# Optimization experiments

Measured on AMD Instinct MI355X. Metric: run time of the kernel, lower is better.

The kernel has to match this reference:

```python
import jax, jax.numpy as jnp
import numpy as np

N, E = 3200, 50000
RBF, HID = 16, 128
CUT = 5.0
NS, NV = 32, 16            # multiplicities of 0e and 1o blocks
D = NS + 3 * NV            # 80 = node/message irrep dim
WNUM = NS*NS + NV*NS + NS*NV + NV*NV  # 2304 tensor-product weights per edge
EPS = 1e-8
# path normalization (fully-connected TP, 2 paths per output irrep)
A1 = 1.0 / np.sqrt(2.0 * NS)
A2 = 1.0 / np.sqrt(2.0 * NV)
A3 = 1.0 / np.sqrt(2.0 * NS)
A4 = 1.0 / np.sqrt(2.0 * NV)
ISQ3 = 1.0 / np.sqrt(3.0)


def setup_inputs() -> dict:
    key = jax.random.key(0)
    ks = jax.random.split(key, 24)
    nrm = lambda k, s, sc=1.0: jax.random.normal(k, s, jnp.float32) * sc
    x = nrm(ks[0], (N, D))
    edge_src = jax.random.randint(ks[1], (E,), 0, N)
    edge_dst = jax.random.randint(ks[2], (E,), 0, N)
    dirs = nrm(ks[3], (E, 3))
    unit = dirs / jnp.linalg.norm(dirs, axis=1, keepdims=True)
    # component-normalized SH for l=0,1: [1, sqrt(3)*r_hat]
    edge_sh = jnp.concatenate([jnp.ones((E, 1), jnp.float32), np.sqrt(3.0) * unit], axis=1)
    edge_rbf = nrm(ks[4], (E, RBF))
    edge_len = jax.random.uniform(ks[5], (E,), jnp.float32, 0.1, 6.0)  # some beyond cutoff
    inp = dict(x=x, edge_src=edge_src, edge_dst=edge_dst, edge_sh=edge_sh,
               edge_rbf=edge_rbf, edge_len=edge_len)
    # IrrepNorm affine params
    inp['norm_w'] = jnp.ones((D,), jnp.float32)
    inp['norm_b'] = jnp.zeros((D,), jnp.float32)
    # radial weight MLP (RBF -> HID -> HID -> WNUM)
    inp['mw1'] = nrm(ks[6], (RBF, HID), 1.0/np.sqrt(RBF)); inp['mb1'] = jnp.zeros((HID,), jnp.float32)
    inp['mw2'] = nrm(ks[7], (HID, HID), 1.0/np.sqrt(HID)); inp['mb2'] = jnp.zeros((HID,), jnp.float32)
    inp['mw3'] = nrm(ks[8], (HID, WNUM), 1.0/np.sqrt(HID)); inp['mb3'] = jnp.zeros((WNUM,), jnp.float32)
    # edge gate MLP (RBF -> HID -> 1)
    inp['gw1'] = nrm(ks[9], (RBF, HID), 1.0/np.sqrt(RBF)); inp['gb1'] = jnp.zeros((HID,), jnp.float32)
    inp['gw2'] = nrm(ks[10], (HID, 1), 1.0/np.sqrt(HID)); inp['gb2'] = jnp.zeros((1,), jnp.float32)
    # equivariant linears (e3nn stores N(0,1) weights, normalizes by 1/sqrt(fan_in))
    inp['Ws'] = nrm(ks[11], (NS, NS + NV))   # msg_linear scalar part: 32 -> 32 scalars + 16 gates
    inp['Wv'] = nrm(ks[12], (NV, NV))        # msg_linear vector part
    inp['Us'] = nrm(ks[13], (NS, NS))        # update_linear
    inp['Uv'] = nrm(ks[14], (NV, NV))
    inp['Ss'] = nrm(ks[15], (NS, NS))        # self_linear
    inp['Sv'] = nrm(ks[16], (NV, NV))
    inp['res_scale'] = jnp.float32(0.1)
    return inp


def _irrep_norm(x, w, b):
    s = x[:, :NS]
    v = x[:, NS:].reshape(-1, NV, 3)
    mean = s.mean(axis=1, keepdims=True)
    var = ((s - mean) ** 2).mean(axis=1, keepdims=True)
    s = (s - mean) / jnp.sqrt(var + EPS)
    rms = jnp.sqrt((v ** 2).mean(axis=2, keepdims=True) + EPS)
    v = v / rms
    out = jnp.concatenate([s, v.reshape(-1, 3 * NV)], axis=-1)
    return out * w + b


def reference(x, edge_src, edge_dst, edge_sh, edge_rbf, edge_len,
              norm_w, norm_b, mw1, mb1, mw2, mb2, mw3, mb3,
              gw1, gb1, gw2, gb2, Ws, Wv, Us, Uv, Ss, Sv, res_scale):
    silu = jax.nn.silu
    x_norm = _irrep_norm(x, norm_w, norm_b)                  # [N, 80]
    # radial tensor-product weights per edge
    h = silu(edge_rbf @ mw1 + mb1)
    h = silu(h @ mw2 + mb2)
    tpw = h @ mw3 + mb3                                      # [E, 2304]
    o1 = NS*NS; o2 = o1 + NV*NS; o3 = o2 + NS*NV
    w1 = tpw[:, :o1].reshape(-1, NS, NS)
    w2 = tpw[:, o1:o2].reshape(-1, NV, NS)
    w3 = tpw[:, o2:o3].reshape(-1, NS, NV)
    w4 = tpw[:, o3:].reshape(-1, NV, NV)
    # gather source node features
    xs = x_norm[edge_src, :NS]                               # [E, 32]
    xv = x_norm[edge_src, NS:].reshape(-1, NV, 3)            # [E, 16, 3]
    sh0 = edge_sh[:, 0]                                      # [E]
    sh1 = edge_sh[:, 1:4]                                    # [E, 3]
    # fully-connected TP paths
    msg_s = A1 * jnp.einsum('ei,eio->eo', xs * sh0[:, None], w1)
    inner = jnp.einsum('eim,em->ei', xv, sh1) * ISQ3         # 1o x 1o -> 0e
    msg_s = msg_s + A2 * jnp.einsum('ei,eio->eo', inner, w2)
    msg_v = A3 * jnp.einsum('ei,eio->eo', xs, w3)[:, :, None] * sh1[:, None, :]
    msg_v = msg_v + A4 * jnp.einsum('eim,eio->eom', xv, w4) * sh0[:, None, None]
    m = jnp.concatenate([msg_s, msg_v.reshape(-1, 3 * NV)], axis=-1)  # [E, 80]
    # cutoff envelope and learned edge gate
    cutoff_w = 0.5 * (jnp.cos(jnp.pi * edge_len / CUT) + 1.0) * (edge_len <= CUT).astype(x.dtype)
    gate_w = jax.nn.sigmoid(silu(edge_rbf @ gw1 + gb1) @ gw2 + gb2)   # [E, 1]
    edge_w = cutoff_w[:, None] * gate_w                               # [E, 1]
    m = m * edge_w
    # scatter-add aggregate + normalization
    agg = jax.ops.segment_sum(m, edge_dst, num_segments=N)            # [N, 80]
    den = jax.ops.segment_sum(edge_w, edge_dst, num_segments=N)       # [N, 1]
    agg = agg / jnp.maximum(den, 1e-8)
    # msg_linear -> scalars + gates + gated vectors
    ag_s = agg[:, :NS]
    ag_v = agg[:, NS:].reshape(-1, NV, 3)
    sc = (ag_s @ Ws) / np.sqrt(NS)                                    # [N, 48]
    vc = jnp.einsum('nim,io->nom', ag_v, Wv) / np.sqrt(NV)            # [N, 16, 3]
    s_g = silu(sc[:, :NS])
    gates = jax.nn.sigmoid(sc[:, NS:])
    v_g = vc * gates[:, :, None]
    # update + self interaction
    upd_s = (s_g @ Us) / np.sqrt(NS)
    upd_v = jnp.einsum('nim,io->nom', v_g, Uv) / np.sqrt(NV)
    self_s = (x_norm[:, :NS] @ Ss) / np.sqrt(NS)
    self_v = jnp.einsum('nim,io->nom', x_norm[:, NS:].reshape(-1, NV, 3), Sv) / np.sqrt(NV)
    out = jnp.concatenate([self_s + upd_s, (self_v + upd_v).reshape(-1, 3 * NV)], axis=-1)
    return x + res_scale * out
```

## Files before the change

### kernel.cpp

```cpp
#include <hip/hip_runtime.h>
#include <hip/hip_bf16.h>
#include <math.h>

#define N_NODES 3200
#define E_EDGES 50000
#define RBFN 16
#define HID 128
#define NS 32
#define NV 16
#define DD 80
#define WNUM 2304
#define CUTF 5.0f
#define EPSF 1e-8f

#define A1C 0.125f
#define A2C 0.17677669529663687f
#define A3C 0.125f
#define A4C 0.17677669529663687f
#define A2ISQ 0.10206207261596575f

typedef __attribute__((ext_vector_type(4))) float f32x4;
typedef __attribute__((ext_vector_type(8))) short bf16x8;

__device__ __forceinline__ float sigm(float x) { return 1.0f / (1.0f + __expf(-x)); }
__device__ __forceinline__ float silu_f(float x) { return x * sigm(x); }

__device__ __forceinline__ short bf16r(float x) {
    union { float f; unsigned u; } v; v.f = x;
    unsigned r = (v.u + 0x7fffu + ((v.u >> 16) & 1u)) >> 16;
    return (short)r;
}
__device__ __forceinline__ float b2f(unsigned short s) {
    union { float f; unsigned u; } v; v.u = ((unsigned)s) << 16; return v.f;
}

__global__ void k_scan(const int* __restrict__ hist, int* __restrict__ start) {
    __shared__ int part[256];
    int t = threadIdx.x;
    int loc[13];
    int s = 0;
#pragma unroll
    for (int j = 0; j < 13; j++) {
        int idx = t * 13 + j;
        int v = (idx < N_NODES) ? hist[idx] : 0;
        loc[j] = s; s += v;
    }
    part[t] = s;
    __syncthreads();
    for (int off = 1; off < 256; off <<= 1) {
        int v = part[t];
        int add = (t >= off) ? part[t - off] : 0;
        __syncthreads();
        part[t] = v + add;
        __syncthreads();
    }
    int pre = (t == 0) ? 0 : part[t - 1];
#pragma unroll
    for (int j = 0; j < 13; j++) {
        int idx = t * 13 + j;
        if (idx < N_NODES) start[idx] = pre + loc[j];
    }
    if (t == 255) start[N_NODES] = part[255];
}

__global__ void k_scatter(const int* __restrict__ edst, const int* __restrict__ start,
                          int* __restrict__ cur, int* __restrict__ perm) {
    int e = blockIdx.x * 256 + threadIdx.x;
    if (e < E_EDGES) {
        int d = edst[e];
        int pos = start[d] + atomicAdd(&cur[d], 1);
        perm[pos] = e;
    }
}

__global__ void k_prep0(const float* __restrict__ mw2, __hip_bfloat16* __restrict__ mw2f) {
    __shared__ __hip_bfloat16 st[2048];
    int t = blockIdx.x, tid = threadIdx.x;
    for (int idx = tid; idx < 2048; idx += 256) {
        int k = idx >> 4, c = idx & 15;
        float v = mw2[k * HID + t * 16 + c];
        int kk = k >> 5, q4 = (k >> 3) & 3, j = k & 7;
        st[kk * 512 + (q4 * 16 + c) * 8 + j] = __float2bfloat16(v);
    }
    __syncthreads();
    ((bf16x8*)(mw2f + t * 2048))[tid] = ((const bf16x8*)st)[tid];
}

__global__ __launch_bounds__(256) void k_front(
    const float* __restrict__ rbf, const float* __restrict__ elen,
    const int* __restrict__ edst,
    const float* __restrict__ mw1, const float* __restrict__ mb1,
    const float* __restrict__ gw1, const float* __restrict__ gb1,
    const float* __restrict__ gw2, const float* __restrict__ gb2,
    const float* __restrict__ mb2, const __hip_bfloat16* __restrict__ mw2f,
    const float* __restrict__ mw3, const float* __restrict__ mb3,
    const float* __restrict__ x, const float* __restrict__ nw, const float* __restrict__ nb,
    float* __restrict__ ewg, __hip_bfloat16* __restrict__ h2b,
    __hip_bfloat16* __restrict__ mw3f, __hip_bfloat16* __restrict__ biasf,
    float* __restrict__ xn, int* __restrict__ hist) {
    __shared__ __align__(16) char smem[16640];
    int b = blockIdx.x, tid = threadIdx.x;
    if (b < 782) {
        __hip_bfloat16* h1l = (__hip_bfloat16*)smem;
        int wid = __builtin_amdgcn_readfirstlane(tid >> 6);
        int lane = tid & 63;
        int base = b * 64;
        int eb = base + wid * 16;
        {
            int c0 = lane, c1 = 64 + lane;
            float t0[16], t1[16], g0[16], g1[16];
            float b0 = mb1[c0], b1 = mb1[c1], gb0v = gb1[c0], gb1v = gb1[c1];
#pragma unroll
            for (int e = 0; e < 16; e++) { t0[e] = b0; t1[e] = b1; g0[e] = gb0v; g1[e] = gb1v; }
#pragma unroll
            for (int r = 0; r < RBFN; r++) {
                float w0 = mw1[r * HID + c0], w1 = mw1[r * HID + c1];
                float v0 = gw1[r * HID + c0], v1 = gw1[r * HID + c1];
#pragma unroll
                for (int e = 0; e < 16; e++) {
                    int ee = eb + e; if (ee >= E_EDGES) ee = E_EDGES - 1;
                    float rv = rbf[ee * RBFN + r];
                    t0[e] += rv * w0; t1[e] += rv * w1;
                    g0[e] += rv * v0; g1[e] += rv * v1;
                }
            }
            float q0 = gw2[c0], q1 = gw2[c1];
            float gb2v = gb2[0];
#pragma unroll
            for (int e = 0; e < 16; e++) {
                int le = wid * 16 + e;
                h1l[le * 128 + c0] = __float2bfloat16(silu_f(t0[e]));
                h1l[le * 128 + c1] = __float2bfloat16(silu_f(t1[e]));
                float p = silu_f(g0[e]) * q0 + silu_f(g1[e]) * q1;
                p += __shfl_xor(p, 1);  p += __shfl_xor(p, 2);  p += __shfl_xor(p, 4);
                p += __shfl_xor(p, 8);  p += __shfl_xor(p, 16); p += __shfl_xor(p, 32);
                if (lane == 0 && eb + e < E_EDGES) {
                    float len = elen[eb + e];
                    float cut = (len <= CUTF) ? 0.5f * (cosf(3.14159265358979f * len / CUTF) + 1.0f) : 0.f;
                    ewg[eb + e] = cut * sigm(p + gb2v);
                }
            }
        }
        __syncthreads();
        {
            int q4 = lane >> 4, l15 = lane & 15;
            int le = wid * 16 + l15;
            bf16x8 af[4];
#pragma unroll
            for (int kk = 0; kk < 4; kk++)
                af[kk] = *(const bf16x8*)(h1l + le * 128 + kk * 32 + q4 * 8);
            const f32x4 zf = {0.f, 0.f, 0.f, 0.f};
#pragma unroll
            for (int ct = 0; ct < 8; ct++) {
                f32x4 acc = zf;
#pragma unroll
                for (int kk = 0; kk < 4; kk++) {
                    bf16x8 bw = *(const bf16x8*)(mw2f + (ct * 4 + kk) * 512 + lane * 8);
                    acc = __builtin_amdgcn_mfma_f32_16x16x32_bf16(af[kk], bw, acc, 0, 0, 0);
                }
                float bias = mb2[ct * 16 + l15];
#pragma unroll
                for (int r = 0; r < 4; r++) {
                    int ge = base + wid * 16 + q4 * 4 + r;
                    if (ge < E_EDGES)
                        h2b[ge * HID + ct * 16 + l15] = __float2bfloat16(silu_f(acc[r] + bias));
                }
            }
        }
    } else if (b < 927) {
        int b2 = b - 782;
        __hip_bfloat16* st = (__hip_bfloat16*)smem;
        if (b2 < 144) {
            for (int idx = tid; idx < 2048; idx += 256) {
                int k = idx >> 4, c = idx & 15;
                float v = mw3[k * WNUM + b2 * 16 + c];
                int kk = k >> 5, q4 = (k >> 3) & 3, j = k & 7;
                st[kk * 512 + (q4 * 16 + c) * 8 + j] = __float2bfloat16(v);
            }
            __syncthreads();
            ((bf16x8*)(mw3f + b2 * 2048))[tid] = ((const bf16x8*)st)[tid];
        } else {
            for (int idx = tid; idx < 3072; idx += 256) {
                float val;
                if (idx < 1024) {
                    int oh = idx >> 9, l = (idx >> 3) & 63, j = idx & 7;
                    int o = oh * 16 + (l & 15), i = (l >> 4) * 8 + j;
                    val = mb3[i * 32 + o];
                } else if (idx < 2048) {
                    int t = idx - 1024;
                    int oh = t >> 9, l = (t >> 3) & 63, j = t & 7;
                    int o = oh * 16 + (l & 15), i = (l >> 4) * 8 + j;
                    val = (i < 16) ? mb3[1024 + i * 32 + o] : 0.f;
                } else if (idx < 2560) {
                    int t = idx - 2048;
                    int l = t >> 3, j = t & 7;
                    int o = l & 15, i = (l >> 4) * 8 + j;
                    val = mb3[1536 + i * 16 + o];
                } else {
                    int t = idx - 2560;
                    int l = t >> 3, j = t & 7;
                    int o = l & 15, i = (l >> 4) * 8 + j;
                    val = (i < 16) ? mb3[2048 + i * 16 + o] : 0.f;
                }
                biasf[idx] = __float2bfloat16(val);
            }
        }
    } else if (b < 1727) {
        float* row = (float*)smem;
        int sub = tid >> 6, t = tid & 63;
        int n = (b - 927) * 4 + sub;
        float* rw = row + sub * 80;
        const float* xr = x + n * DD;
        rw[t] = xr[t];
        if (t < 16) rw[64 + t] = xr[64 + t];
        __syncthreads();
        float mean = 0.f;
#pragma unroll
        for (int i = 0; i < NS; i++) mean += rw[i];
        mean *= (1.0f / NS);
        float var = 0.f;
#pragma unroll
        for (int i = 0; i < NS; i++) { float d = rw[i] - mean; var += d * d; }
        var *= (1.0f / NS);
        float inv = rsqrtf(var + EPSF);
        if (t < NS) xn[n * DD + t] = (rw[t] - mean) * inv * nw[t] + nb[t];
        if (t < 48) {
            int j = t / 3;
            float v0 = rw[NS + 3 * j], v1 = rw[NS + 3 * j + 1], v2 = rw[NS + 3 * j + 2];
            float rms = sqrtf((v0 * v0 + v1 * v1 + v2 * v2) * (1.0f / 3.0f) + EPSF);
            xn[n * DD + NS + t] = rw[NS + t] / rms * nw[NS + t] + nb[NS + t];
        }
    } else {
        int e = (b - 1727) * 256 + tid;
        if (e < E_EDGES) atomicAdd(&hist[edst[e]], 1);
    }
}

__global__ __launch_bounds__(128) void k_msg(
    const float* __restrict__ xn, const __hip_bfloat16* __restrict__ h2b,
    const float* __restrict__ ewg, const int* __restrict__ esrc,
    const int* __restrict__ edst, const int* __restrict__ perm,
    const float* __restrict__ esh,
    const __hip_bfloat16* __restrict__ mw3f, const __hip_bfloat16* __restrict__ biasf,
    const int* __restrict__ startp, float* __restrict__ agg, float* __restrict__ den) {
    __shared__ __align__(16) char pool[29696];
    unsigned short (*xng)[82]  = (unsigned short(*)[82])(pool);
    unsigned short (*innr)[16] = (unsigned short(*)[16])(pool + 20992);
    float (*sh1l)[4] = (float(*)[4])(pool + 25088);
    float* sh0l = (float*)(pool + 27136);
    float* ewl  = (float*)(pool + 27648);
    int* dstl   = (int*)(pool + 28160);
    int* srcl   = (int*)(pool + 28672);
    int* gel    = (int*)(pool + 29184);
    float* msgl = (float*)pool;

    const int tid = threadIdx.x;
    const int wid = __builtin_amdgcn_readfirstlane(tid >> 6);
    const int lane = tid & 63;
    const int q4 = lane >> 4;
    const int l15 = lane & 15;
    const int ib = q4 * 8;
    const int role = blockIdx.x & 1;
    const int e0 = (blockIdx.x >> 1) * 128;

    if (tid < 128) {
        int slot = e0 + tid;
        bool v = slot < E_EDGES;
        int ge = v ? perm[slot] : 0;
        gel[tid] = ge;
        srcl[tid] = esrc[ge];
        dstl[tid] = v ? edst[ge] : -1;
        ewl[tid] = v ? ewg[ge] : 0.f;
        sh0l[tid] = esh[ge * 4];
        sh1l[tid][0] = esh[ge * 4 + 1];
        sh1l[tid][1] = esh[ge * 4 + 2];
        sh1l[tid][2] = esh[ge * 4 + 3];
    }
    __syncthreads();
    for (int idx = tid; idx < 128 * 80; idx += 128) {
        int e = idx / 80, q = idx - e * 80;
        xng[e][q] = (unsigned short)bf16r(xn[srcl[e] * 80 + q]);
    }
    __syncthreads();
    for (int idx = tid; idx < 128 * 16; idx += 128) {
        int e = idx >> 4, i = idx & 15;
        float d = b2f(xng[e][32 + 3 * i]) * sh1l[e][0]
                + b2f(xng[e][32 + 3 * i + 1]) * sh1l[e][1]
                + b2f(xng[e][32 + 3 * i + 2]) * sh1l[e][2];
        innr[e][i] = (unsigned short)bf16r(A2ISQ * d);
    }
    __syncthreads();

    int el[4];
#pragma unroll
    for (int et = 0; et < 4; et++) el[et] = wid * 64 + et * 16 + l15;
    bf16x8 hfr[4][4];
#pragma unroll
    for (int et = 0; et < 4; et++) {
        int ge = gel[el[et]];
        const __hip_bfloat16* hr = h2b + ge * HID;
#pragma unroll
        for (int kk = 0; kk < 4; kk++)
            hfr[et][kk] = *(const bf16x8*)(hr + kk * 32 + ib);
    }
    const f32x4 zf = {0.f, 0.f, 0.f, 0.f};
    const bf16x8* gp = (const bf16x8*)mw3f;
    int cnt = E_EDGES - e0; if (cnt > 128) cnt = 128;

    if (role == 0) {
        float f1[4];
        f32x4 msgS[2][4];
#pragma unroll
        for (int et = 0; et < 4; et++) {
            f1[et] = A1C * sh0l[el[et]];
            bf16x8 p18, p28;
#pragma unroll
            for (int j = 0; j < 8; j++) {
                p18[j] = bf16r(b2f(xng[el[et]][ib + j]) * f1[et]);
                p28[j] = (ib + j < 16) ? (short)innr[el[et]][ib + j] : (short)0;
            }
            bf16x8 ba1a = *(const bf16x8*)(biasf + lane * 8);
            bf16x8 ba1b = *(const bf16x8*)(biasf + 512 + lane * 8);
            bf16x8 ba2a = *(const bf16x8*)(biasf + 1024 + lane * 8);
            bf16x8 ba2b = *(const bf16x8*)(biasf + 1536 + lane * 8);
            f32x4 a0 = __builtin_amdgcn_mfma_f32_16x16x32_bf16(ba1a, p18, zf, 0, 0, 0);
            msgS[0][et] = __builtin_amdgcn_mfma_f32_16x16x32_bf16(ba2a, p28, a0, 0, 0, 0);
            f32x4 a1 = __builtin_amdgcn_mfma_f32_16x16x32_bf16(ba1b, p18, zf, 0, 0, 0);
            msgS[1][et] = __builtin_amdgcn_mfma_f32_16x16x32_bf16(ba2b, p28, a1, 0, 0, 0);
        }
        auto computeA = [&](int n, bf16x8 (&A)[8]) {
            f32x4 acc[2][4];
#pragma unroll
            for (int half = 0; half < 2; half++)
#pragma unroll
                for (int et = 0; et < 4; et++) acc[half][et] = zf;
#pragma unroll
            for (int half = 0; half < 2; half++)
#pragma unroll
                for (int kk = 0; kk < 4; kk++)
#pragma unroll
                    for (int et = 0; et < 4; et++)
                        acc[half][et] = __builtin_amdgcn_mfma_f32_16x16x32_bf16(
                            A[half * 4 + kk], hfr[et][kk], acc[half][et], 0, 0, 0);
            float p[4];
            if (n < 32) {
#pragma unroll
                for (int et = 0; et < 4; et++) p[et] = f1[et] * b2f(xng[el[et]][n]);
            } else {
#pragma unroll
                for (int et = 0; et < 4; et++) p[et] = b2f(innr[el[et]][n - 32]);
            }
#pragma unroll
            for (int half = 0; half < 2; half++)
#pragma unroll
                for (int et = 0; et < 4; et++)
#pragma unroll
                    for (int r = 0; r < 4; r++)
                        msgS[half][et][r] += p[et] * acc[half][et][r];
        };
        bf16x8 A0[8], A1[8];
#pragma unroll
        for (int f = 0; f < 8; f++) A0[f] = gp[f * 64 + lane];
        for (int n = 0; n < 48; n += 2) {
            const bf16x8* g1 = gp + (n + 1) * 512;
#pragma unroll
            for (int f = 0; f < 8; f++) A1[f] = g1[f * 64 + lane];
            computeA(n, A0);
            if (n + 2 < 48) {
                const bf16x8* g2 = gp + (n + 2) * 512;
#pragma unroll
                for (int f = 0; f < 8; f++) A0[f] = g2[f * 64 + lane];
            }
            computeA(n + 1, A1);
        }
        __syncthreads();
#pragma unroll
        for (int et = 0; et < 4; et++) {
            int le = el[et];
            float ew = ewl[le];
#pragma unroll
            for (int oh = 0; oh < 2; oh++)
#pragma unroll
                for (int r = 0; r < 4; r++)
                    msgl[le * 48 + oh * 16 + q4 * 4 + r] = msgS[oh][et][r] * ew;
        }
        __syncthreads();
        if (tid < 33) {
            int c = tid;
            int cur = dstl[0];
            float acc = 0.f;
            for (int r = 0; r < cnt; r++) {
                int nd = dstl[r];
                if (nd != cur) {
                    if (cur >= 0) {
                        bool interior = (startp[cur] >= e0) && (startp[cur + 1] <= e0 + 128);
                        float* p = (c == 32) ? (den + cur) : (agg + cur * 80 + c);
                        if (interior) *p = acc; else atomicAdd(p, acc);
                    }
                    acc = 0.f; cur = nd;
                }
                acc += (c == 32) ? ewl[r] : msgl[r * 48 + c];
            }
            if (cur >= 0) {
                bool interior = (startp[cur] >= e0) && (startp[cur + 1] <= e0 + 128);
                float* p = (c == 32) ? (den + cur) : (agg + cur * 80 + c);
                if (interior) *p = acc; else atomicAdd(p, acc);
            }
        }
    } else {
        float f4e[4];
        f32x4 q3[4], qv[3][4];
#pragma unroll
        for (int et = 0; et < 4; et++) {
            f4e[et] = A4C * sh0l[el[et]];
            bf16x8 xs8;
#pragma unroll
            for (int j = 0; j < 8; j++) xs8[j] = (short)xng[el[et]][ib + j];
            bf16x8 ba3 = *(const bf16x8*)(biasf + 2048 + lane * 8);
            bf16x8 ba4 = *(const bf16x8*)(biasf + 2560 + lane * 8);
            q3[et] = __builtin_amdgcn_mfma_f32_16x16x32_bf16(ba3, xs8, zf, 0, 0, 0);
#pragma unroll
            for (int m = 0; m < 3; m++) {
                bf16x8 t8;
#pragma unroll
                for (int j = 0; j < 8; j++) {
                    int i = ib + j;
                    t8[j] = (i < 16) ? (short)xng[el[et]][32 + 3 * i + m] : (short)0;
                }
                qv[m][et] = __builtin_amdgcn_mfma_f32_16x16x32_bf16(ba4, t8, zf, 0, 0, 0);
            }
        }
        auto computeB = [&](int n, bf16x8 (&A)[8]) {
            f32x4 acc[2][4];
#pragma unroll
            for (int half = 0; half < 2; half++)
#pragma unroll
                for (int et = 0; et < 4; et++) acc[half][et] = zf;
#pragma unroll
            for (int half = 0; half < 2; half++)
#pragma unroll
                for (int kk = 0; kk < 4; kk++)
#pragma unroll
                    for (int et = 0; et < 4; et++)
                        acc[half][et] = __builtin_amdgcn_mfma_f32_16x16x32_bf16(
                            A[half * 4 + kk], hfr[et][kk], acc[half][et], 0, 0, 0);
            if (n < 64) {
#pragma unroll
                for (int half = 0; half < 2; half++) {
                    int i = 2 * (n - 48) + half;
                    float p[4];
#pragma unroll
                    for (int et = 0; et < 4; et++) p[et] = b2f(xng[el[et]][i]);
#pragma unroll
                    for (int et = 0; et < 4; et++)
#pragma unroll
                        for (int r = 0; r < 4; r++)
                            q3[et][r] += p[et] * acc[half][et][r];
                }
            } else {
#pragma unroll
                for (int half = 0; half < 2; half++) {
                    int i = 2 * (n - 64) + half;
#pragma unroll
                    for (int m = 0; m < 3; m++) {
                        float p[4];
#pragma unroll
                        for (int et = 0; et < 4; et++) p[et] = b2f(xng[el[et]][32 + 3 * i + m]);
#pragma unroll
                        for (int et = 0; et < 4; et++)
#pragma unroll
                            for (int r = 0; r < 4; r++)
                                qv[m][et][r] += p[et] * acc[half][et][r];
                    }
                }
            }
        };
        bf16x8 A0[8], A1[8];
#pragma unroll
        for (int f = 0; f < 8; f++) A0[f] = gp[48 * 512 + f * 64 + lane];
        for (int n = 48; n < 72; n += 2) {
            const bf16x8* g1 = gp + (n + 1) * 512;
#pragma unroll
            for (int f = 0; f < 8; f++) A1[f] = g1[f * 64 + lane];
            computeB(n, A0);
            if (n + 2 < 72) {
                const bf16x8* g2 = gp + (n + 2) * 512;
#pragma unroll
                for (int f = 0; f < 8; f++) A0[f] = g2[f * 64 + lane];
            }
            computeB(n + 1, A1);
        }
        __syncthreads();
#pragma unroll
        for (int et = 0; et < 4; et++) {
            int le = el[et];
            float ew = ewl[le];
            float s0 = sh1l[le][0], s1 = sh1l[le][1], s2 = sh1l[le][2];
            float b4 = f4e[et];
#pragma unroll
            for (int r = 0; r < 4; r++) {
                int o = q4 * 4 + r;
                float qq = A3C * q3[et][r];
                msgl[le * 48 + o * 3 + 0] = (qq * s0 + b4 * qv[0][et][r]) * ew;
                msgl[le * 48 + o * 3 + 1] = (qq * s1 + b4 * qv[1][et][r]) * ew;
                msgl[le * 48 + o * 3 + 2] = (qq * s2 + b4 * qv[2][et][r]) * ew;
            }
        }
        __syncthreads();
        if (tid < 48) {
            int c = tid;
            int cur = dstl[0];
            float acc = 0.f;
            for (int r = 0; r < cnt; r++) {
                int nd = dstl[r];
                if (nd != cur) {
                    if (cur >= 0) {
                        bool interior = (startp[cur] >= e0) && (startp[cur + 1] <= e0 + 128);
                        float* p = agg + cur * 80 + 32 + c;
                        if (interior) *p = acc; else atomicAdd(p, acc);
                    }
                    acc = 0.f; cur = nd;
                }
                acc += msgl[r * 48 + c];
            }
            if (cur >= 0) {
                bool interior = (startp[cur] >= e0) && (startp[cur + 1] <= e0 + 128);
                float* p = agg + cur * 80 + 32 + c;
                if (interior) *p = acc; else atomicAdd(p, acc);
            }
        }
    }
}

__global__ void k_update(
    const float* __restrict__ x, const float* __restrict__ xn,
    const float* __restrict__ agg, const float* __restrict__ den,
    const float* __restrict__ Ws, const float* __restrict__ Wv,
    const float* __restrict__ Us, const float* __restrict__ Uv,
    const float* __restrict__ Ss, const float* __restrict__ Sv,
    const float* __restrict__ rsp, float* __restrict__ out) {
    int n = blockIdx.x, t = threadIdx.x;
    __shared__ float ag[DD];
    __shared__ float xnl[DD];
    __shared__ float sg[NS];
    __shared__ float gt[NV];
    __shared__ float vg[48];
    float idv = 1.0f / fmaxf(den[n], 1e-8f);
    ag[t] = agg[n * DD + t] * idv;
    if (t < 16) ag[64 + t] = agg[n * DD + 64 + t] * idv;
    xnl[t] = xn[n * DD + t];
    if (t < 16) xnl[64 + t] = xn[n * DD + 64 + t];
    __syncthreads();
    const float iqs = 0.17677669529663687f;
    const float iqv = 0.25f;
    if (t < 48) {
        float acc = 0.f;
#pragma unroll
        for (int i = 0; i < NS; i++) acc += ag[i] * Ws[i * 48 + t];
        acc *= iqs;
        if (t < NS) sg[t] = silu_f(acc);
        else gt[t - NS] = sigm(acc);
    }
    __syncthreads();
    if (t < 48) {
        int o = t / 3, m = t - 3 * o;
        float acc = 0.f;
#pragma unroll
        for (int i = 0; i < NV; i++) acc += ag[NS + 3 * i + m] * Wv[i * NV + o];
        vg[t] = acc * iqv * gt[o];
    }
    __syncthreads();
    float rs = rsp[0];
    if (t < NS) {
        float us = 0.f, ss = 0.f;
#pragma unroll
        for (int i = 0; i < NS; i++) { us += sg[i] * Us[i * NS + t]; ss += xnl[i] * Ss[i * NS + t]; }
        out[n * DD + t] = x[n * DD + t] + rs * ((ss + us) * iqs);
    }
    if (t < 48) {
        int o = t / 3, m = t - 3 * o;
        float uv = 0.f, sv = 0.f;
#pragma unroll
        for (int i = 0; i < NV; i++) { uv += vg[3 * i + m] * Uv[i * NV + o]; sv += xnl[NS + 3 * i + m] * Sv[i * NV + o]; }
        out[n * DD + NS + t] = x[n * DD + NS + t] + rs * ((sv + uv) * iqv);
    }
}

extern "C" void kernel_launch(void* const* d_in, const int* in_sizes, int n_in,
                              void* d_out, int out_size, void* d_ws, size_t ws_size,
                              hipStream_t stream) {
    (void)in_sizes; (void)n_in; (void)out_size; (void)ws_size;
    const float* x    = (const float*)d_in[0];
    const int*   esrc = (const int*)d_in[1];
    const int*   edst = (const int*)d_in[2];
    const float* esh  = (const float*)d_in[3];
    const float* erbf = (const float*)d_in[4];
    const float* elen = (const float*)d_in[5];
    const float* nw   = (const float*)d_in[6];
    const float* nb   = (const float*)d_in[7];
    const float* mw1  = (const float*)d_in[8];
    const float* mb1  = (const float*)d_in[9];
    const float* mw2  = (const float*)d_in[10];
    const float* mb2  = (const float*)d_in[11];
    const float* mw3  = (const float*)d_in[12];
    const float* mb3  = (const float*)d_in[13];
    const float* gw1  = (const float*)d_in[14];
    const float* gb1  = (const float*)d_in[15];
    const float* gw2  = (const float*)d_in[16];
    const float* gb2  = (const float*)d_in[17];
    const float* Ws   = (const float*)d_in[18];
    const float* Wv   = (const float*)d_in[19];
    const float* Us   = (const float*)d_in[20];
    const float* Uv   = (const float*)d_in[21];
    const float* Ss   = (const float*)d_in[22];
    const float* Sv   = (const float*)d_in[23];
    const float* rsp  = (const float*)d_in[24];
    float* out = (float*)d_out;
    float* ws  = (float*)d_ws;

    float* agg    = ws;
    float* den    = ws + 256000;
    int*   hist   = (int*)(ws + 259200);
    int*   cur    = (int*)(ws + 262400);
    int*   startp = (int*)(ws + 265600);
    int*   perm   = (int*)(ws + 268801);
    float* xn     = ws + 318804;
    float* ewg    = ws + 574804;
    __hip_bfloat16* h2b   = (__hip_bfloat16*)(ws + 624804);
    __hip_bfloat16* mw3f  = (__hip_bfloat16*)(ws + 3824804);
    __hip_bfloat16* biasf = (__hip_bfloat16*)(ws + 3972260);
    __hip_bfloat16* mw2f  = (__hip_bfloat16*)(ws + 3973796);

    hipMemsetAsync(ws, 0, 265600 * sizeof(float), stream);
    k_prep0<<<8, 256, 0, stream>>>(mw2, mw2f);
    k_front<<<1923, 256, 0, stream>>>(erbf, elen, edst, mw1, mb1, gw1, gb1, gw2, gb2,
                                      mb2, mw2f, mw3, mb3, x, nw, nb,
                                      ewg, h2b, mw3f, biasf, xn, hist);
    k_scan<<<1, 256, 0, stream>>>(hist, startp);
    k_scatter<<<196, 256, 0, stream>>>(edst, startp, cur, perm);
    k_msg<<<782, 128, 0, stream>>>(xn, h2b, ewg, esrc, edst, perm, esh,
                                   mw3f, biasf, startp, agg, den);
    k_update<<<N_NODES, 64, 0, stream>>>(x, xn, agg, den, Ws, Wv, Us, Uv, Ss, Sv, rsp, out);
}
```

Baseline: 269.4 us.

## Split message kernel weight-row loop across six blocks per edge tile

The message kernel previously used two blocks per 128-edge tile (scalar and vector outputs), each looping over 48 or 24 weight rows. It now launches six blocks per tile, each handling 12 weight rows, and gathers only the node-feature columns its slice needs. The segmented reduction is spread over both waves and always uses atomics because partial sums now come from several blocks. This gives more parallelism on a grid that had only 782 blocks. In exchange, the h2b fragment loads and source gathers are repeated per slice, and atomic traffic on agg rises.

```diff
diff --git a/kernel.cpp b/kernel.cpp
--- a/kernel.cpp
+++ b/kernel.cpp
@@ -260,8 +260,9 @@
     const int q4 = lane >> 4;
     const int l15 = lane & 15;
     const int ib = q4 * 8;
-    const int role = blockIdx.x & 1;
-    const int e0 = (blockIdx.x >> 1) * 128;
+    const int grp = blockIdx.x / 6;
+    const int slice = blockIdx.x - 6 * grp;
+    const int e0 = grp * 128;
 
     if (tid < 128) {
         int slot = e0 + tid;
@@ -277,17 +278,49 @@
         sh1l[tid][2] = esh[ge * 4 + 3];
     }
     __syncthreads();
-    for (int idx = tid; idx < 128 * 80; idx += 128) {
-        int e = idx / 80, q = idx - e * 80;
-        xng[e][q] = (unsigned short)bf16r(xn[srcl[e] * 80 + q]);
-    }
-    __syncthreads();
-    for (int idx = tid; idx < 128 * 16; idx += 128) {
-        int e = idx >> 4, i = idx & 15;
-        float d = b2f(xng[e][32 + 3 * i]) * sh1l[e][0]
-                + b2f(xng[e][32 + 3 * i + 1]) * sh1l[e][1]
-                + b2f(xng[e][32 + 3 * i + 2]) * sh1l[e][2];
-        innr[e][i] = (unsigned short)bf16r(A2ISQ * d);
+    if (slice == 0 || slice == 4) {
+        for (int idx = tid; idx < 128 * 32; idx += 128) {
+            int e = idx >> 5, q = idx & 31;
+            xng[e][q] = (unsigned short)bf16r(xn[srcl[e] * 80 + q]);
+        }
+    } else if (slice == 1) {
+        for (int idx = tid; idx < 128 * 12; idx += 128) {
+            int e = idx / 12, q = 12 + (idx - e * 12);
+            xng[e][q] = (unsigned short)bf16r(xn[srcl[e] * 80 + q]);
+        }
+    } else if (slice == 2) {
+        for (int idx = tid; idx < 128 * 20; idx += 128) {
+            int e = idx / 20, q = 24 + (idx - e * 20);
+            xng[e][q] = (unsigned short)bf16r(xn[srcl[e] * 80 + q]);
+        }
+    } else if (slice == 3) {
+        for (int idx = tid; idx < 128 * 48; idx += 128) {
+            int e = idx / 48, q = 32 + (idx - e * 48);
+            xng[e][q] = (unsigned short)bf16r(xn[srcl[e] * 80 + q]);
+        }
+    } else {
+        for (int idx = tid; idx < 128 * 56; idx += 128) {
+            int e = idx / 56, q = 24 + (idx - e * 56);
+            xng[e][q] = (unsigned short)bf16r(xn[srcl[e] * 80 + q]);
+        }
+    }
+    __syncthreads();
+    if (slice == 2) {
+        for (int idx = tid; idx < 128 * 4; idx += 128) {
+            int e = idx >> 2, i = idx & 3;
+            float d = b2f(xng[e][32 + 3 * i]) * sh1l[e][0]
+                    + b2f(xng[e][32 + 3 * i + 1]) * sh1l[e][1]
+                    + b2f(xng[e][32 + 3 * i + 2]) * sh1l[e][2];
+            innr[e][i] = (unsigned short)bf16r(A2ISQ * d);
+        }
+    } else if (slice == 3) {
+        for (int idx = tid; idx < 128 * 16; idx += 128) {
+            int e = idx >> 4, i = idx & 15;
+            float d = b2f(xng[e][32 + 3 * i]) * sh1l[e][0]
+                    + b2f(xng[e][32 + 3 * i + 1]) * sh1l[e][1]
+                    + b2f(xng[e][32 + 3 * i + 2]) * sh1l[e][2];
+            innr[e][i] = (unsigned short)bf16r(A2ISQ * d);
+        }
     }
     __syncthreads();
 
@@ -307,26 +340,34 @@
     const bf16x8* gp = (const bf16x8*)mw3f;
     int cnt = E_EDGES - e0; if (cnt > 128) cnt = 128;
 
-    if (role == 0) {
+    if (slice < 4) {
+        const int nlo = slice * 12, nhi = nlo + 12;
         float f1[4];
         f32x4 msgS[2][4];
 #pragma unroll
         for (int et = 0; et < 4; et++) {
             f1[et] = A1C * sh0l[el[et]];
-            bf16x8 p18, p28;
-#pragma unroll
-            for (int j = 0; j < 8; j++) {
-                p18[j] = bf16r(b2f(xng[el[et]][ib + j]) * f1[et]);
-                p28[j] = (ib + j < 16) ? (short)innr[el[et]][ib + j] : (short)0;
-            }
-            bf16x8 ba1a = *(const bf16x8*)(biasf + lane * 8);
-            bf16x8 ba1b = *(const bf16x8*)(biasf + 512 + lane * 8);
-            bf16x8 ba2a = *(const bf16x8*)(biasf + 1024 + lane * 8);
-            bf16x8 ba2b = *(const bf16x8*)(biasf + 1536 + lane * 8);
-            f32x4 a0 = __builtin_amdgcn_mfma_f32_16x16x32_bf16(ba1a, p18, zf, 0, 0, 0);
-            msgS[0][et] = __builtin_amdgcn_mfma_f32_16x16x32_bf16(ba2a, p28, a0, 0, 0, 0);
-            f32x4 a1 = __builtin_amdgcn_mfma_f32_16x16x32_bf16(ba1b, p18, zf, 0, 0, 0);
-            msgS[1][et] = __builtin_amdgcn_mfma_f32_16x16x32_bf16(ba2b, p28, a1, 0, 0, 0);
+            if (slice == 0) {
+                bf16x8 p18;
+#pragma unroll
+                for (int j = 0; j < 8; j++)
+                    p18[j] = bf16r(b2f(xng[el[et]][ib + j]) * f1[et]);
+                bf16x8 ba1a = *(const bf16x8*)(biasf + lane * 8);
+                bf16x8 ba1b = *(const bf16x8*)(biasf + 512 + lane * 8);
+                msgS[0][et] = __builtin_amdgcn_mfma_f32_16x16x32_bf16(ba1a, p18, zf, 0, 0, 0);
+                msgS[1][et] = __builtin_amdgcn_mfma_f32_16x16x32_bf16(ba1b, p18, zf, 0, 0, 0);
+            } else if (slice == 3) {
+                bf16x8 p28;
+#pragma unroll
+                for (int j = 0; j < 8; j++)
+                    p28[j] = (ib + j < 16) ? (short)innr[el[et]][ib + j] : (short)0;
+                bf16x8 ba2a = *(const bf16x8*)(biasf + 1024 + lane * 8);
+                bf16x8 ba2b = *(const bf16x8*)(biasf + 1536 + lane * 8);
+                msgS[0][et] = __builtin_amdgcn_mfma_f32_16x16x32_bf16(ba2a, p28, zf, 0, 0, 0);
+                msgS[1][et] = __builtin_amdgcn_mfma_f32_16x16x32_bf16(ba2b, p28, zf, 0, 0, 0);
+            } else {
+                msgS[0][et] = zf; msgS[1][et] = zf;
+            }
         }
         auto computeA = [&](int n, bf16x8 (&A)[8]) {
             f32x4 acc[2][4];
@@ -359,14 +400,17 @@
                         msgS[half][et][r] += p[et] * acc[half][et][r];
         };
         bf16x8 A0[8], A1[8];
-#pragma unroll
-        for (int f = 0; f < 8; f++) A0[f] = gp[f * 64 + lane];
-        for (int n = 0; n < 48; n += 2) {
+        {
+            const bf16x8* g0 = gp + nlo * 512;
+#pragma unroll
+            for (int f = 0; f < 8; f++) A0[f] = g0[f * 64 + lane];
+        }
+        for (int n = nlo; n < nhi; n += 2) {
             const bf16x8* g1 = gp + (n + 1) * 512;
 #pragma unroll
             for (int f = 0; f < 8; f++) A1[f] = g1[f * 64 + lane];
             computeA(n, A0);
-            if (n + 2 < 48) {
+            if (n + 2 < nhi) {
                 const bf16x8* g2 = gp + (n + 2) * 512;
 #pragma unroll
                 for (int f = 0; f < 8; f++) A0[f] = g2[f * 64 + lane];
@@ -385,49 +429,55 @@
                     msgl[le * 48 + oh * 16 + q4 * 4 + r] = msgS[oh][et][r] * ew;
         }
         __syncthreads();
-        if (tid < 33) {
-            int c = tid;
-            int cur = dstl[0];
-            float acc = 0.f;
-            for (int r = 0; r < cnt; r++) {
-                int nd = dstl[r];
-                if (nd != cur) {
-                    if (cur >= 0) {
-                        bool interior = (startp[cur] >= e0) && (startp[cur + 1] <= e0 + 128);
-                        float* p = (c == 32) ? (den + cur) : (agg + cur * 80 + c);
-                        if (interior) *p = acc; else atomicAdd(p, acc);
+        {
+            int nch = (slice == 0) ? 33 : 32;
+            int c = lane;
+            int r0 = wid * 64;
+            int rend = (cnt < r0 + 64) ? cnt : (r0 + 64);
+            if (c < nch && r0 < cnt) {
+                int cur = dstl[r0];
+                float acc = 0.f;
+                for (int r = r0; r < rend; r++) {
+                    int nd = dstl[r];
+                    if (nd != cur) {
+                        if (cur >= 0)
+                            atomicAdd((c == 32) ? (den + cur) : (agg + cur * 80 + c), acc);
+                        acc = 0.f; cur = nd;
                     }
-                    acc = 0.f; cur = nd;
-                }
-                acc += (c == 32) ? ewl[r] : msgl[r * 48 + c];
-            }
-            if (cur >= 0) {
-                bool interior = (startp[cur] >= e0) && (startp[cur + 1] <= e0 + 128);
-                float* p = (c == 32) ? (den + cur) : (agg + cur * 80 + c);
-                if (interior) *p = acc; else atomicAdd(p, acc);
+                    acc += (c == 32) ? ewl[r] : msgl[r * 48 + c];
+                }
+                if (cur >= 0)
+                    atomicAdd((c == 32) ? (den + cur) : (agg + cur * 80 + c), acc);
             }
         }
     } else {
+        const int nlo = 48 + (slice - 4) * 12, nhi = nlo + 12;
         float f4e[4];
         f32x4 q3[4], qv[3][4];
 #pragma unroll
         for (int et = 0; et < 4; et++) {
             f4e[et] = A4C * sh0l[el[et]];
-            bf16x8 xs8;
-#pragma unroll
-            for (int j = 0; j < 8; j++) xs8[j] = (short)xng[el[et]][ib + j];
-            bf16x8 ba3 = *(const bf16x8*)(biasf + 2048 + lane * 8);
-            bf16x8 ba4 = *(const bf16x8*)(biasf + 2560 + lane * 8);
-            q3[et] = __builtin_amdgcn_mfma_f32_16x16x32_bf16(ba3, xs8, zf, 0, 0, 0);
-#pragma unroll
-            for (int m = 0; m < 3; m++) {
-                bf16x8 t8;
-#pragma unroll
-                for (int j = 0; j < 8; j++) {
-                    int i = ib + j;
-                    t8[j] = (i < 16) ? (short)xng[el[et]][32 + 3 * i + m] : (short)0;
-                }
-                qv[m][et] = __builtin_amdgcn_mfma_f32_16x16x32_bf16(ba4, t8, zf, 0, 0, 0);
+            if (slice == 4) {
+                bf16x8 xs8;
+#pragma unroll
+                for (int j = 0; j < 8; j++) xs8[j] = (short)xng[el[et]][ib + j];
+                bf16x8 ba3 = *(const bf16x8*)(biasf + 2048 + lane * 8);
+                q3[et] = __builtin_amdgcn_mfma_f32_16x16x32_bf16(ba3, xs8, zf, 0, 0, 0);
+#pragma unroll
+                for (int m = 0; m < 3; m++) qv[m][et] = zf;
+            } else {
+                q3[et] = zf;
+                bf16x8 ba4 = *(const bf16x8*)(biasf + 2560 + lane * 8);
+#pragma unroll
+                for (int m = 0; m < 3; m++) {
+                    bf16x8 t8;
+#pragma unroll
+                    for (int j = 0; j < 8; j++) {
+                        int i = ib + j;
+                        t8[j] = (i < 16) ? (short)xng[el[et]][32 + 3 * i + m] : (short)0;
+                    }
+                    qv[m][et] = __builtin_amdgcn_mfma_f32_16x16x32_bf16(ba4, t8, zf, 0, 0, 0);
+                }
             }
         }
         auto computeB = [&](int n, bf16x8 (&A)[8]) {
@@ -476,14 +526,17 @@
             }
         };
         bf16x8 A0[8], A1[8];
-#pragma unroll
-        for (int f = 0; f < 8; f++) A0[f] = gp[48 * 512 + f * 64 + lane];
-        for (int n = 48; n < 72; n += 2) {
+        {
+            const bf16x8* g0 = gp + nlo * 512;
+#pragma unroll
+            for (int f = 0; f < 8; f++) A0[f] = g0[f * 64 + lane];
+        }
+        for (int n = nlo; n < nhi; n += 2) {
             const bf16x8* g1 = gp + (n + 1) * 512;
 #pragma unroll
             for (int f = 0; f < 8; f++) A1[f] = g1[f * 64 + lane];
             computeB(n, A0);
-            if (n + 2 < 72) {
+            if (n + 2 < nhi) {
                 const bf16x8* g2 = gp + (n + 2) * 512;
 #pragma unroll
                 for (int f = 0; f < 8; f++) A0[f] = g2[f * 64 + lane];
@@ -507,26 +560,22 @@
             }
         }
         __syncthreads();
-        if (tid < 48) {
-            int c = tid;
-            int cur = dstl[0];
-            float acc = 0.f;
-            for (int r = 0; r < cnt; r++) {
-                int nd = dstl[r];
-                if (nd != cur) {
-                    if (cur >= 0) {
-                        bool interior = (startp[cur] >= e0) && (startp[cur + 1] <= e0 + 128);
-                        float* p = agg + cur * 80 + 32 + c;
-                        if (interior) *p = acc; else atomicAdd(p, acc);
+        {
+            int c = lane;
+            int r0 = wid * 64;
+            int rend = (cnt < r0 + 64) ? cnt : (r0 + 64);
+            if (c < 48 && r0 < cnt) {
+                int cur = dstl[r0];
+                float acc = 0.f;
+                for (int r = r0; r < rend; r++) {
+                    int nd = dstl[r];
+                    if (nd != cur) {
+                        if (cur >= 0) atomicAdd(agg + cur * 80 + 32 + c, acc);
+                        acc = 0.f; cur = nd;
                     }
-                    acc = 0.f; cur = nd;
-                }
-                acc += msgl[r * 48 + c];
-            }
-            if (cur >= 0) {
-                bool interior = (startp[cur] >= e0) && (startp[cur + 1] <= e0 + 128);
-                float* p = agg + cur * 80 + 32 + c;
-                if (interior) *p = acc; else atomicAdd(p, acc);
+                    acc += msgl[r * 48 + c];
+                }
+                if (cur >= 0) atomicAdd(agg + cur * 80 + 32 + c, acc);
             }
         }
     }
@@ -638,7 +687,7 @@
                                       ewg, h2b, mw3f, biasf, xn, hist);
     k_scan<<<1, 256, 0, stream>>>(hist, startp);
     k_scatter<<<196, 256, 0, stream>>>(edst, startp, cur, perm);
-    k_msg<<<782, 128, 0, stream>>>(xn, h2b, ewg, esrc, edst, perm, esh,
-                                   mw3f, biasf, startp, agg, den);
+    k_msg<<<2346, 128, 0, stream>>>(xn, h2b, ewg, esrc, edst, perm, esh,
+                                    mw3f, biasf, startp, agg, den);
     k_update<<<N_NODES, 64, 0, stream>>>(x, xn, agg, den, Ws, Wv, Us, Uv, Ss, Sv, rsp, out);
 }
```

After: 322.9 us. 19.9% more time.
